# Performance work log

Hardware: AMD Instinct MI355X
Metric: run time of the kernel (lower is better)

## Reference

```python
import jax, jax.numpy as jnp
import numpy as np

D_MODEL = 1024
N_HEADS = 16
D_HEAD = 64
GROUP_SIZE = 2
N_GROUPS = N_HEADS // GROUP_SIZE


def setup_inputs() -> dict:
    key = jax.random.key(0)
    k1, k2, k3, k4, k5 = jax.random.split(key, 5)
    def xavier(k, shape):
        fan_in, fan_out = shape[0], int(np.prod(shape[1:]))
        bound = float(np.sqrt(6.0 / (fan_in + fan_out)))
        return jax.random.uniform(k, shape, jnp.float32, -bound, bound)
    return {
        'resid': jax.random.normal(k1, (2, 2048, D_MODEL), jnp.float32),
        'W_Q': xavier(k2, (D_MODEL, N_HEADS, D_HEAD)),
        'W_K': xavier(k3, (D_MODEL, N_GROUPS, D_HEAD)),
        'W_V': xavier(k4, (D_MODEL, N_GROUPS, D_HEAD)),
        'W_out': xavier(k5, (D_HEAD, N_HEADS, D_MODEL)),
        'b_out': jnp.zeros((D_MODEL,), jnp.float32),
    }


def reference(resid, W_Q, W_K, W_V, W_out, b_out):
    batch, seq, _ = resid.shape
    # q: [b, s, n_heads, d_head] -> [b, s, n_groups, group_size, d_head]
    q = jnp.einsum('bsd,dhe->bshe', resid, W_Q)
    q = q.reshape(batch, seq, N_GROUPS, GROUP_SIZE, D_HEAD)
    k = jnp.einsum('bsd,dge->bsge', resid, W_K)  # [b, s, g, e]
    v = jnp.einsum('bsd,dge->bsge', resid, W_V)
    # scores: [b, g, group_size, qseq, kseq]
    scores = jnp.einsum('bqgre,bkge->bgrqk', q, k) / jnp.sqrt(jnp.float32(D_HEAD))
    causal_mask = jnp.triu(jnp.ones((seq, seq), bool), k=1)
    scores = jnp.where(causal_mask, jnp.float32(-1000000.0), scores)
    probs = jax.nn.softmax(scores, axis=-1)
    # z: [b, q, g, r, e]
    z = jnp.einsum('bgrqk,bkge->bqgre', probs, v)
    z = z.reshape(batch, seq, N_HEADS, D_HEAD)
    out = jnp.einsum('bshe,ehd->bsd', z, W_out) + b_out
    return out
```

## Files before the change

kernel.cpp:

```cpp
#include <hip/hip_runtime.h>

#define BATCH   2
#define SEQ     2048
#define DMODEL  1024
#define NHEADS  16
#define DHEAD   64
#define NGROUPS 8
#define NTOK    (BATCH * SEQ)
#define QKV_N   2048

typedef unsigned short ushort_t;
typedef unsigned int u32;
typedef __attribute__((ext_vector_type(8))) short short8;
typedef __attribute__((ext_vector_type(4))) float f32x4;
typedef __attribute__((ext_vector_type(16))) float f32x16;

#define MFMA16(a, b, c) __builtin_amdgcn_mfma_f32_16x16x32_bf16((a), (b), (c), 0, 0, 0)
#define MFMA32(a, b, c) __builtin_amdgcn_mfma_f32_32x32x16_bf16((a), (b), (c), 0, 0, 0)

#define GLOAD16(gp, lp)                                                        \
    __builtin_amdgcn_global_load_lds(                                          \
        (const u32 __attribute__((address_space(1)))*)(gp),                    \
        (u32 __attribute__((address_space(3)))*)(lp), 16, 0, 0)

#define CVTPK(dst, lo, hi) \
    asm("v_cvt_pk_bf16_f32 %0, %1, %2" : "=v"(dst) : "v"(lo), "v"(hi))

#define PLSWAP(a, b) \
    asm("v_permlane32_swap_b32 %0, %1" : "+v"(a), "+v"(b))

__device__ __forceinline__ ushort_t f2bu(float x) {
    unsigned u = __builtin_bit_cast(unsigned, x);
    unsigned r = (u + 0x7fffu + ((u >> 16) & 1u)) >> 16;
    return (ushort_t)r;
}

__global__ __launch_bounds__(256) void prep(
    const float* __restrict__ resid,
    const float* __restrict__ Wq, const float* __restrict__ Wk,
    const float* __restrict__ Wv, const float* __restrict__ Wout,
    ushort_t* __restrict__ rbf, ushort_t* __restrict__ Wt,
    ushort_t* __restrict__ Wot)
{
    __shared__ float Ws[64][65];
    const int t = threadIdx.x;
    const int bid = blockIdx.x;

    if (bid < 4096) {
        const int i4 = bid * 256 + t;
        union { float4 v; float f[4]; } a;
        a.v = *reinterpret_cast<const float4*>(resid + (size_t)i4 * 4);
        union { uint2 v; ushort_t u[4]; } o;
        #pragma unroll
        for (int j = 0; j < 4; ++j) o.u[j] = f2bu(a.f[j]);
        *reinterpret_cast<uint2*>(rbf + (size_t)i4 * 4) = o.v;
        return;
    }

    if (bid < 4096 + 512) {
        const int rel = bid - 4096;
        const int k0 = (rel & 15) * 64;
        const int n0 = (rel >> 4) * 64;

        const float* src; int stride, boff;
        if (n0 < 1024)       { src = Wq; stride = 1024; boff = n0; }
        else if (n0 < 1536)  { src = Wk; stride = 512;  boff = n0 - 1024; }
        else                 { src = Wv; stride = 512;  boff = n0 - 1536; }

        #pragma unroll
        for (int i = 0; i < 4; ++i) {
            const int c = i * 256 + t;
            const int row = c >> 4, cc = (c & 15) * 4;
            union { float4 v; float f[4]; } a;
            a.v = *reinterpret_cast<const float4*>(
                src + (size_t)(k0 + row) * stride + boff + cc);
            #pragma unroll
            for (int j = 0; j < 4; ++j) Ws[row][cc + j] = a.f[j];
        }
        __syncthreads();
        #pragma unroll
        for (int i = 0; i < 2; ++i) {
            const int c = i * 256 + t;
            const int nr = c >> 3, kc = (c & 7) * 8;
            union { uint4 v; ushort_t u[8]; } o;
            #pragma unroll
            for (int j = 0; j < 8; ++j) o.u[j] = f2bu(Ws[kc + j][nr]);
            *reinterpret_cast<uint4*>(Wt + (size_t)(n0 + nr) * 1024 + k0 + kc) = o.v;
        }
        return;
    }

    {
        const int rel = bid - 4608;
        const int d0 = (rel & 15) * 64;
        const int h  = rel >> 4;

        #pragma unroll
        for (int i = 0; i < 4; ++i) {
            const int c = i * 256 + t;
            const int e = c >> 4, dd = (c & 15) * 4;
            union { float4 v; float f[4]; } a;
            a.v = *reinterpret_cast<const float4*>(
                Wout + (size_t)(e * 16 + h) * 1024 + d0 + dd);
            #pragma unroll
            for (int j = 0; j < 4; ++j) Ws[e][dd + j] = a.f[j];
        }
        __syncthreads();
        #pragma unroll
        for (int i = 0; i < 2; ++i) {
            const int c = i * 256 + t;
            const int dr = c >> 3, ec = (c & 7) * 8;
            union { uint4 v; ushort_t u[8]; } o;
            #pragma unroll
            for (int j = 0; j < 8; ++j) o.u[j] = f2bu(Ws[ec + j][dr]);
            *reinterpret_cast<uint4*>(Wot + (size_t)(d0 + dr) * 1024 + h * 64 + ec) = o.v;
        }
    }
}

__global__ __launch_bounds__(256) void tr_v(
    const ushort_t* __restrict__ qkv, ushort_t* __restrict__ Vt)
{
    __shared__ ushort_t T[64][72];
    const int t  = threadIdx.x;
    const int s0 = blockIdx.x * 64;
    const int g  = blockIdx.y;
    const int b  = blockIdx.z;

    #pragma unroll
    for (int i = 0; i < 2; ++i) {
        const int c = i * 256 + t;
        const int row = c >> 3, ec = (c & 7) * 8;
        *reinterpret_cast<uint4*>(&T[row][ec]) =
            *reinterpret_cast<const uint4*>(
                qkv + (size_t)(b * SEQ + s0 + row) * QKV_N + 1536 + g * 64 + ec);
    }
    __syncthreads();
    #pragma unroll
    for (int i = 0; i < 2; ++i) {
        const int c = i * 256 + t;
        const int er = c >> 3, sc = (c & 7) * 8;
        union { uint4 v; ushort_t u[8]; } o;
        #pragma unroll
        for (int j = 0; j < 8; ++j) o.u[j] = T[sc + j][er];
        *reinterpret_cast<uint4*>(
            Vt + (size_t)((b * NGROUPS + g) * 64 + er) * SEQ + s0 + sc) = o.v;
    }
}

__global__ __launch_bounds__(512) void qkv_gemm(
    const ushort_t* __restrict__ A, const ushort_t* __restrict__ Bt,
    ushort_t* __restrict__ C)
{
    __shared__ ushort_t As[2][128][64];
    __shared__ ushort_t Bs[2][128][64];

    const int t = threadIdx.x;
    const int wave = t >> 6, lane = t & 63;
    const int quad = lane >> 4, x = lane & 15;
    const int wm = (wave >> 1) * 32, wn = (wave & 1) * 64;
    const int m0 = blockIdx.y * 128, n0 = blockIdx.x * 128;

    const int sr8 = lane >> 3;
    const int gc  = (lane & 7) ^ sr8;

    f32x4 acc[2][4];
    #pragma unroll
    for (int i = 0; i < 2; ++i)
        #pragma unroll
        for (int j = 0; j < 4; ++j) acc[i][j] = (f32x4)(0.f);

    #pragma unroll
    for (int s = 0; s < 2; ++s) {
        const int r0 = (wave * 2 + s) * 8;
        GLOAD16(A  + (size_t)(m0 + r0 + sr8) * 1024 + gc * 8, &As[0][r0][0]);
        GLOAD16(Bt + (size_t)(n0 + r0 + sr8) * 1024 + gc * 8, &Bs[0][r0][0]);
    }
    __syncthreads();

    int cur = 0;
    for (int k0 = 0; k0 < 1024; k0 += 64) {
        if (k0 + 64 < 1024) {
            #pragma unroll
            for (int s = 0; s < 2; ++s) {
                const int r0 = (wave * 2 + s) * 8;
                GLOAD16(A  + (size_t)(m0 + r0 + sr8) * 1024 + k0 + 64 + gc * 8,
                        &As[cur ^ 1][r0][0]);
                GLOAD16(Bt + (size_t)(n0 + r0 + sr8) * 1024 + k0 + 64 + gc * 8,
                        &Bs[cur ^ 1][r0][0]);
            }
        }
        #pragma unroll
        for (int j = 0; j < 2; ++j) {
            const int cs = ((j * 4 + quad) ^ (x & 7)) * 8;
            short8 af[2], bf[4];
            #pragma unroll
            for (int mt = 0; mt < 2; ++mt)
                af[mt] = *reinterpret_cast<const short8*>(&As[cur][wm + mt * 16 + x][cs]);
            #pragma unroll
            for (int nt = 0; nt < 4; ++nt)
                bf[nt] = *reinterpret_cast<const short8*>(&Bs[cur][wn + nt * 16 + x][cs]);
            #pragma unroll
            for (int mt = 0; mt < 2; ++mt)
                #pragma unroll
                for (int nt = 0; nt < 4; ++nt)
                    acc[mt][nt] = MFMA16(af[mt], bf[nt], acc[mt][nt]);
        }
        __syncthreads();
        cur ^= 1;
    }

    #pragma unroll
    for (int mt = 0; mt < 2; ++mt)
        #pragma unroll
        for (int nt = 0; nt < 4; ++nt)
            #pragma unroll
            for (int r = 0; r < 4; ++r) {
                const int row = m0 + wm + mt * 16 + quad * 4 + r;
                const int col = n0 + wn + nt * 16 + x;
                C[(size_t)row * QKV_N + col] = f2bu(acc[mt][nt][r]);
            }
}

__global__ __launch_bounds__(512) void out_gemm(
    const ushort_t* __restrict__ A, const ushort_t* __restrict__ Bt,
    const float* __restrict__ bias, float* __restrict__ C)
{
    __shared__ ushort_t As[2][128][64];
    __shared__ ushort_t Bs[2][64][64];

    const int t = threadIdx.x;
    const int wave = t >> 6, lane = t & 63;
    const int quad = lane >> 4, x = lane & 15;
    const int wm = (wave >> 1) * 32, wn = (wave & 1) * 32;
    const int m0 = blockIdx.y * 128, n0 = blockIdx.x * 64;

    const int sr8 = lane >> 3;
    const int gc  = (lane & 7) ^ sr8;

    f32x4 acc[2][2];
    #pragma unroll
    for (int i = 0; i < 2; ++i)
        #pragma unroll
        for (int j = 0; j < 2; ++j) acc[i][j] = (f32x4)(0.f);

    #pragma unroll
    for (int s = 0; s < 2; ++s) {
        const int r0 = (wave * 2 + s) * 8;
        GLOAD16(A + (size_t)(m0 + r0 + sr8) * 1024 + gc * 8, &As[0][r0][0]);
    }
    {
        const int r0 = wave * 8;
        GLOAD16(Bt + (size_t)(n0 + r0 + sr8) * 1024 + gc * 8, &Bs[0][r0][0]);
    }
    __syncthreads();

    int cur = 0;
    for (int k0 = 0; k0 < 1024; k0 += 64) {
        if (k0 + 64 < 1024) {
            #pragma unroll
            for (int s = 0; s < 2; ++s) {
                const int r0 = (wave * 2 + s) * 8;
                GLOAD16(A + (size_t)(m0 + r0 + sr8) * 1024 + k0 + 64 + gc * 8,
                        &As[cur ^ 1][r0][0]);
            }
            const int r0 = wave * 8;
            GLOAD16(Bt + (size_t)(n0 + r0 + sr8) * 1024 + k0 + 64 + gc * 8,
                    &Bs[cur ^ 1][r0][0]);
        }
        #pragma unroll
        for (int j = 0; j < 2; ++j) {
            const int cs = ((j * 4 + quad) ^ (x & 7)) * 8;
            short8 af[2], bf[2];
            #pragma unroll
            for (int mt = 0; mt < 2; ++mt)
                af[mt] = *reinterpret_cast<const short8*>(&As[cur][wm + mt * 16 + x][cs]);
            #pragma unroll
            for (int nt = 0; nt < 2; ++nt)
                bf[nt] = *reinterpret_cast<const short8*>(&Bs[cur][wn + nt * 16 + x][cs]);
            #pragma unroll
            for (int mt = 0; mt < 2; ++mt)
                #pragma unroll
                for (int nt = 0; nt < 2; ++nt)
                    acc[mt][nt] = MFMA16(af[mt], bf[nt], acc[mt][nt]);
        }
        __syncthreads();
        cur ^= 1;
    }

    float bv[2];
    #pragma unroll
    for (int nt = 0; nt < 2; ++nt) bv[nt] = bias[n0 + wn + nt * 16 + x];

    #pragma unroll
    for (int mt = 0; mt < 2; ++mt)
        #pragma unroll
        for (int nt = 0; nt < 2; ++nt)
            #pragma unroll
            for (int r = 0; r < 4; ++r) {
                const int row = m0 + wm + mt * 16 + quad * 4 + r;
                const int col = n0 + wn + nt * 16 + x;
                C[(size_t)row * 1024 + col] = acc[mt][nt][r] + bv[nt];
            }
}

__global__ __launch_bounds__(512, 4) void attn(
    const ushort_t* __restrict__ qkv, const ushort_t* __restrict__ Vt,
    ushort_t* __restrict__ z)
{
    __shared__ ushort_t smem[4 * 128 * 64];
    ushort_t (*Ks)[128][64]  = (ushort_t(*)[128][64])(smem);
    ushort_t (*Vts)[64][128] = (ushort_t(*)[64][128])(smem + 2 * 128 * 64);
    float* Ob1  = (float*)smem;
    float* Ob3  = (float*)(smem + 128 * 64);
    float* Ofin = (float*)(smem + 2 * 128 * 64);
    float* Lb1  = (float*)(smem + 3 * 128 * 64);
    float* Lb3  = Lb1 + 64;

    const int t = threadIdx.x;
    const int wave = t >> 6, lane = t & 63;
    const int x31 = lane & 31, hi = lane >> 5;
    const int rw = wave & 1;
    const int kw = wave >> 1;

    const int h  = blockIdx.x;
    const int qp = blockIdx.y;
    const int b  = blockIdx.z;
    const int g  = h >> 1;

    const int krow = t >> 3;
    const int kc   = t & 7;
    const int vrow = t >> 4;
    const int vc   = t & 15;

    const ushort_t* kgb = qkv + (size_t)(b * SEQ) * QKV_N + 1024 + g * 64 + kc * 8;
    const ushort_t* vgb = Vt + (size_t)((b * NGROUPS + g) * 64) * SEQ + vc * 8;

    const int kswz = (kc ^ (krow & 7)) * 8;
    const int vswz = (vc ^ (vrow & 15)) * 8;

    const int qloc = rw * 32 + x31;

    #pragma unroll
    for (int phase = 0; phase < 2; ++phase) {
        const int qt = phase ? (31 - qp) : qp;
        const int qrow0 = qt * 64;
        const int nkt = (qt >> 1) + 1;

        short8 aq[4];
        #pragma unroll
        for (int sl = 0; sl < 4; ++sl)
            aq[sl] = *reinterpret_cast<const short8*>(
                qkv + (size_t)(b * SEQ + qrow0 + qloc) * QKV_N + h * 64 + sl * 16 + hi * 8);

        f32x16 o0 = (f32x16)(0.f), o1 = (f32x16)(0.f);
        float lown = 0.f;

        __syncthreads();

        {
            uint4 a0 = *reinterpret_cast<const uint4*>(kgb + (size_t)krow * QKV_N);
            uint4 a1 = *reinterpret_cast<const uint4*>(kgb + (size_t)(krow + 64) * QKV_N);
            uint4 b0 = *reinterpret_cast<const uint4*>(vgb + (size_t)vrow * SEQ);
            uint4 b1 = *reinterpret_cast<const uint4*>(vgb + (size_t)(vrow + 32) * SEQ);
            *reinterpret_cast<uint4*>(&Ks[0][krow][kswz])       = a0;
            *reinterpret_cast<uint4*>(&Ks[0][krow + 64][kswz])  = a1;
            *reinterpret_cast<uint4*>(&Vts[0][vrow][vswz])      = b0;
            *reinterpret_cast<uint4*>(&Vts[0][vrow + 32][vswz]) = b1;
        }
        __syncthreads();

        for (int kt = 0; kt < nkt; ++kt) {
            const int cur = kt & 1;
            const bool more = (kt + 1 < nkt);

            uint4 a0, a1, b0, b1;
            if (more) {
                const size_t kb = (size_t)((kt + 1) * 128);
                a0 = *reinterpret_cast<const uint4*>(kgb + (kb + krow) * QKV_N);
                a1 = *reinterpret_cast<const uint4*>(kgb + (kb + krow + 64) * QKV_N);
                b0 = *reinterpret_cast<const uint4*>(vgb + (size_t)vrow * SEQ + kb);
                b1 = *reinterpret_cast<const uint4*>(vgb + (size_t)(vrow + 32) * SEQ + kb);
            }

            const int cbase = kt * 128 + kw * 32;
            const int qmin  = qrow0 + rw * 32;

            if (cbase <= qmin + 31) {
                const bool full = (cbase + 31 <= qmin);

                f32x16 st = (f32x16)(0.f);
                __builtin_amdgcn_s_setprio(1);
                #pragma unroll
                for (int sl = 0; sl < 4; ++sl) {
                    short8 ak = *reinterpret_cast<const short8*>(
                        &Ks[cur][kw * 32 + x31][((sl * 2 + hi) ^ (x31 & 7)) * 8]);
                    st = MFMA32(ak, aq[sl], st);
                }
                __builtin_amdgcn_s_setprio(0);

                const int ql = qmin + x31 - cbase;
                float p[16];
                float s16 = 0.f;
                #pragma unroll
                for (int r = 0; r < 16; ++r) {
                    const int keyoff = (r & 3) + 8 * (r >> 2);
                    float pv = __expf(st[r] * 0.125f);
                    if (!full) pv = (keyoff + 4 * hi > ql) ? 0.f : pv;
                    p[r] = pv;
                    s16 += pv;
                }
                lown += s16;

                u32 pk0, pk1, pk2, pk3, pk4, pk5, pk6, pk7;
                CVTPK(pk0, p[0],  p[1]);  CVTPK(pk1, p[2],  p[3]);
                CVTPK(pk2, p[4],  p[5]);  CVTPK(pk3, p[6],  p[7]);
                CVTPK(pk4, p[8],  p[9]);  CVTPK(pk5, p[10], p[11]);
                CVTPK(pk6, p[12], p[13]); CVTPK(pk7, p[14], p[15]);
                PLSWAP(pk0, pk2); PLSWAP(pk1, pk3);
                PLSWAP(pk4, pk6); PLSWAP(pk5, pk7);
                union { u32 u[4]; short8 s; } f0, f1;
                f0.u[0] = pk0; f0.u[1] = pk1; f0.u[2] = pk2; f0.u[3] = pk3;
                f1.u[0] = pk4; f1.u[1] = pk5; f1.u[2] = pk6; f1.u[3] = pk7;

                __builtin_amdgcn_s_setprio(1);
                #pragma unroll
                for (int ks = 0; ks < 2; ++ks) {
                    const short8 pf = ks ? f1.s : f0.s;
                    short8 av0 = *reinterpret_cast<const short8*>(
                        &Vts[cur][x31][((kw * 4 + ks * 2 + hi) ^ (x31 & 15)) * 8]);
                    o0 = MFMA32(av0, pf, o0);
                    short8 av1 = *reinterpret_cast<const short8*>(
                        &Vts[cur][32 + x31][((kw * 4 + ks * 2 + hi) ^ (x31 & 15)) * 8]);
                    o1 = MFMA32(av1, pf, o1);
                }
                __builtin_amdgcn_s_setprio(0);
            }

            if (more) {
                *reinterpret_cast<uint4*>(&Ks[cur ^ 1][krow][kswz])       = a0;
                *reinterpret_cast<uint4*>(&Ks[cur ^ 1][krow + 64][kswz])  = a1;
                *reinterpret_cast<uint4*>(&Vts[cur ^ 1][vrow][vswz])      = b0;
                *reinterpret_cast<uint4*>(&Vts[cur ^ 1][vrow + 32][vswz]) = b1;
            }
            __syncthreads();
        }

        float ltot;
        {
            u32 la = __builtin_bit_cast(u32, lown), lb = la;
            PLSWAP(la, lb);
            const float lpart = __builtin_bit_cast(float, hi ? la : lb);
            ltot = lown + lpart;
        }

        if (kw == 1 || kw == 3) {
            float* Obx = (kw == 1) ? Ob1 : Ob3;
            float* Lbx = (kw == 1) ? Lb1 : Lb3;
            #pragma unroll
            for (int r = 0; r < 16; ++r) {
                const int e = (r & 3) + 8 * (r >> 2) + 4 * hi;
                Obx[e * 64 + qloc]        = o0[r];
                Obx[(32 + e) * 64 + qloc] = o1[r];
            }
            if (hi == 0) Lbx[qloc] = ltot;
        }
        __syncthreads();
        if (kw == 0 || kw == 2) {
            const float* Obx = (kw == 0) ? Ob1 : Ob3;
            const float* Lbx = (kw == 0) ? Lb1 : Lb3;
            #pragma unroll
            for (int r = 0; r < 16; ++r) {
                const int e = (r & 3) + 8 * (r >> 2) + 4 * hi;
                o0[r] += Obx[e * 64 + qloc];
                o1[r] += Obx[(32 + e) * 64 + qloc];
            }
            ltot += Lbx[qloc];
        }
        __syncthreads();
        if (kw == 2) {
            #pragma unroll
            for (int r = 0; r < 16; ++r) {
                const int e = (r & 3) + 8 * (r >> 2) + 4 * hi;
                Ob1[e * 64 + qloc]        = o0[r];
                Ob1[(32 + e) * 64 + qloc] = o1[r];
            }
            if (hi == 0) Lb1[qloc] = ltot;
        }
        __syncthreads();
        if (kw == 0) {
            #pragma unroll
            for (int r = 0; r < 16; ++r) {
                const int e = (r & 3) + 8 * (r >> 2) + 4 * hi;
                o0[r] += Ob1[e * 64 + qloc];
                o1[r] += Ob1[(32 + e) * 64 + qloc];
            }
            ltot += Lb1[qloc];
            const float inv = 1.f / ltot;
            #pragma unroll
            for (int r = 0; r < 16; ++r) {
                const int e = (r & 3) + 8 * (r >> 2) + 4 * hi;
                Ofin[e * 64 + qloc]        = o0[r] * inv;
                Ofin[(32 + e) * 64 + qloc] = o1[r] * inv;
            }
        }
        __syncthreads();

        {
            const int q = t >> 3, ec = t & 7;
            union { u32 u[4]; uint4 v; } pkz;
            #pragma unroll
            for (int j2 = 0; j2 < 4; ++j2) {
                float v0 = Ofin[(ec * 8 + 2 * j2) * 64 + q];
                float v1 = Ofin[(ec * 8 + 2 * j2 + 1) * 64 + q];
                CVTPK(pkz.u[j2], v0, v1);
            }
            *reinterpret_cast<uint4*>(
                z + (size_t)(b * SEQ + qrow0 + q) * 1024 + h * 64 + ec * 8) = pkz.v;
        }
    }
}

extern "C" void kernel_launch(void* const* d_in, const int* in_sizes, int n_in,
                              void* d_out, int out_size, void* d_ws, size_t ws_size,
                              hipStream_t stream)
{
    const float* resid = (const float*)d_in[0];
    const float* Wq    = (const float*)d_in[1];
    const float* Wk    = (const float*)d_in[2];
    const float* Wv    = (const float*)d_in[3];
    const float* Wout  = (const float*)d_in[4];
    const float* bout  = (const float*)d_in[5];
    float* out = (float*)d_out;

    ushort_t* rbf   = (ushort_t*)d_ws;
    ushort_t* wqkvt = rbf   + (size_t)NTOK * DMODEL;
    ushort_t* woutt = wqkvt + (size_t)QKV_N * DMODEL;
    ushort_t* qkv   = woutt + (size_t)DMODEL * DMODEL;
    ushort_t* z     = qkv   + (size_t)NTOK * QKV_N;
    ushort_t* vt    = rbf;

    prep     <<<dim3(4864), 256, 0, stream>>>(resid, Wq, Wk, Wv, Wout,
                                              rbf, wqkvt, woutt);
    qkv_gemm <<<dim3(16, 32), 512, 0, stream>>>(rbf, wqkvt, qkv);
    tr_v     <<<dim3(SEQ / 64, NGROUPS, BATCH), 256, 0, stream>>>(qkv, vt);
    attn     <<<dim3(16, 16, 2), 512, 0, stream>>>(qkv, vt, z);
    out_gemm <<<dim3(16, 32), 512, 0, stream>>>(z, woutt, bout, out);
}
```

Baseline: 164.5 us.

## Load K/V fragments directly from global memory instead of staging through LDS

The attention kernel no longer stages K and V tiles through double-buffered shared memory with per-tile barriers. Each wave now loads its own K and V MFMA fragments straight from global memory into registers and skips masked tiles early. This removes LDS traffic and the __syncthreads per key tile. In exchange, fragments shared across waves are fetched redundantly from global/L2, and there is no explicit prefetch to hide load latency.

```diff
diff --git a/kernel.cpp b/kernel.cpp
--- a/kernel.cpp
+++ b/kernel.cpp
@@ -308,14 +308,11 @@
     const ushort_t* __restrict__ qkv, const ushort_t* __restrict__ Vt,
     ushort_t* __restrict__ z)
 {
-    __shared__ ushort_t smem[4 * 128 * 64];
-    ushort_t (*Ks)[128][64]  = (ushort_t(*)[128][64])(smem);
-    ushort_t (*Vts)[64][128] = (ushort_t(*)[64][128])(smem + 2 * 128 * 64);
-    float* Ob1  = (float*)smem;
-    float* Ob3  = (float*)(smem + 128 * 64);
-    float* Ofin = (float*)(smem + 2 * 128 * 64);
-    float* Lb1  = (float*)(smem + 3 * 128 * 64);
-    float* Lb3  = Lb1 + 64;
+    __shared__ float Ob1[64 * 64];
+    __shared__ float Ob3[64 * 64];
+    __shared__ float Ofin[64 * 64];
+    __shared__ float Lb1[64];
+    __shared__ float Lb3[64];
 
     const int t = threadIdx.x;
     const int wave = t >> 6, lane = t & 63;
@@ -328,16 +325,8 @@
     const int b  = blockIdx.z;
     const int g  = h >> 1;
 
-    const int krow = t >> 3;
-    const int kc   = t & 7;
-    const int vrow = t >> 4;
-    const int vc   = t & 15;
-
-    const ushort_t* kgb = qkv + (size_t)(b * SEQ) * QKV_N + 1024 + g * 64 + kc * 8;
-    const ushort_t* vgb = Vt + (size_t)((b * NGROUPS + g) * 64) * SEQ + vc * 8;
-
-    const int kswz = (kc ^ (krow & 7)) * 8;
-    const int vswz = (vc ^ (vrow & 15)) * 8;
+    const ushort_t* kg = qkv + (size_t)(b * SEQ) * QKV_N + 1024 + g * 64;
+    const ushort_t* vg = Vt + (size_t)((b * NGROUPS + g) * 64) * SEQ;
 
     const int qloc = rw * 32 + x31;
 
@@ -356,94 +345,67 @@
         f32x16 o0 = (f32x16)(0.f), o1 = (f32x16)(0.f);
         float lown = 0.f;
 
-        __syncthreads();
-
-        {
-            uint4 a0 = *reinterpret_cast<const uint4*>(kgb + (size_t)krow * QKV_N);
-            uint4 a1 = *reinterpret_cast<const uint4*>(kgb + (size_t)(krow + 64) * QKV_N);
-            uint4 b0 = *reinterpret_cast<const uint4*>(vgb + (size_t)vrow * SEQ);
-            uint4 b1 = *reinterpret_cast<const uint4*>(vgb + (size_t)(vrow + 32) * SEQ);
-            *reinterpret_cast<uint4*>(&Ks[0][krow][kswz])       = a0;
-            *reinterpret_cast<uint4*>(&Ks[0][krow + 64][kswz])  = a1;
-            *reinterpret_cast<uint4*>(&Vts[0][vrow][vswz])      = b0;
-            *reinterpret_cast<uint4*>(&Vts[0][vrow + 32][vswz]) = b1;
-        }
-        __syncthreads();
-
         for (int kt = 0; kt < nkt; ++kt) {
-            const int cur = kt & 1;
-            const bool more = (kt + 1 < nkt);
-
-            uint4 a0, a1, b0, b1;
-            if (more) {
-                const size_t kb = (size_t)((kt + 1) * 128);
-                a0 = *reinterpret_cast<const uint4*>(kgb + (kb + krow) * QKV_N);
-                a1 = *reinterpret_cast<const uint4*>(kgb + (kb + krow + 64) * QKV_N);
-                b0 = *reinterpret_cast<const uint4*>(vgb + (size_t)vrow * SEQ + kb);
-                b1 = *reinterpret_cast<const uint4*>(vgb + (size_t)(vrow + 32) * SEQ + kb);
-            }
-
             const int cbase = kt * 128 + kw * 32;
             const int qmin  = qrow0 + rw * 32;
-
-            if (cbase <= qmin + 31) {
-                const bool full = (cbase + 31 <= qmin);
-
-                f32x16 st = (f32x16)(0.f);
-                __builtin_amdgcn_s_setprio(1);
-                #pragma unroll
-                for (int sl = 0; sl < 4; ++sl) {
-                    short8 ak = *reinterpret_cast<const short8*>(
-                        &Ks[cur][kw * 32 + x31][((sl * 2 + hi) ^ (x31 & 7)) * 8]);
-                    st = MFMA32(ak, aq[sl], st);
-                }
-                __builtin_amdgcn_s_setprio(0);
-
-                const int ql = qmin + x31 - cbase;
-                float p[16];
-                float s16 = 0.f;
-                #pragma unroll
-                for (int r = 0; r < 16; ++r) {
-                    const int keyoff = (r & 3) + 8 * (r >> 2);
-                    float pv = __expf(st[r] * 0.125f);
-                    if (!full) pv = (keyoff + 4 * hi > ql) ? 0.f : pv;
-                    p[r] = pv;
-                    s16 += pv;
-                }
-                lown += s16;
-
-                u32 pk0, pk1, pk2, pk3, pk4, pk5, pk6, pk7;
-                CVTPK(pk0, p[0],  p[1]);  CVTPK(pk1, p[2],  p[3]);
-                CVTPK(pk2, p[4],  p[5]);  CVTPK(pk3, p[6],  p[7]);
-                CVTPK(pk4, p[8],  p[9]);  CVTPK(pk5, p[10], p[11]);
-                CVTPK(pk6, p[12], p[13]); CVTPK(pk7, p[14], p[15]);
-                PLSWAP(pk0, pk2); PLSWAP(pk1, pk3);
-                PLSWAP(pk4, pk6); PLSWAP(pk5, pk7);
-                union { u32 u[4]; short8 s; } f0, f1;
-                f0.u[0] = pk0; f0.u[1] = pk1; f0.u[2] = pk2; f0.u[3] = pk3;
-                f1.u[0] = pk4; f1.u[1] = pk5; f1.u[2] = pk6; f1.u[3] = pk7;
-
-                __builtin_amdgcn_s_setprio(1);
-                #pragma unroll
-                for (int ks = 0; ks < 2; ++ks) {
-                    const short8 pf = ks ? f1.s : f0.s;
-                    short8 av0 = *reinterpret_cast<const short8*>(
-                        &Vts[cur][x31][((kw * 4 + ks * 2 + hi) ^ (x31 & 15)) * 8]);
-                    o0 = MFMA32(av0, pf, o0);
-                    short8 av1 = *reinterpret_cast<const short8*>(
-                        &Vts[cur][32 + x31][((kw * 4 + ks * 2 + hi) ^ (x31 & 15)) * 8]);
-                    o1 = MFMA32(av1, pf, o1);
-                }
-                __builtin_amdgcn_s_setprio(0);
-            }
-
-            if (more) {
-                *reinterpret_cast<uint4*>(&Ks[cur ^ 1][krow][kswz])       = a0;
-                *reinterpret_cast<uint4*>(&Ks[cur ^ 1][krow + 64][kswz])  = a1;
-                *reinterpret_cast<uint4*>(&Vts[cur ^ 1][vrow][vswz])      = b0;
-                *reinterpret_cast<uint4*>(&Vts[cur ^ 1][vrow + 32][vswz]) = b1;
-            }
-            __syncthreads();
+            if (cbase > qmin + 31) continue;
+            const bool full = (cbase + 31 <= qmin);
+
+            short8 kf[4];
+            #pragma unroll
+            for (int sl = 0; sl < 4; ++sl)
+                kf[sl] = *reinterpret_cast<const short8*>(
+                    kg + (size_t)(cbase + x31) * QKV_N + sl * 16 + hi * 8);
+
+            short8 vf0[2], vf1[2];
+            #pragma unroll
+            for (int ks = 0; ks < 2; ++ks) {
+                const size_t vcol = (size_t)(kt * 128 + (kw * 4 + ks * 2 + hi) * 8);
+                vf0[ks] = *reinterpret_cast<const short8*>(
+                    vg + (size_t)x31 * SEQ + vcol);
+                vf1[ks] = *reinterpret_cast<const short8*>(
+                    vg + (size_t)(32 + x31) * SEQ + vcol);
+            }
+
+            f32x16 st = (f32x16)(0.f);
+            __builtin_amdgcn_s_setprio(1);
+            #pragma unroll
+            for (int sl = 0; sl < 4; ++sl)
+                st = MFMA32(kf[sl], aq[sl], st);
+            __builtin_amdgcn_s_setprio(0);
+
+            const int ql = qmin + x31 - cbase;
+            float p[16];
+            float s16 = 0.f;
+            #pragma unroll
+            for (int r = 0; r < 16; ++r) {
+                const int keyoff = (r & 3) + 8 * (r >> 2);
+                float pv = __expf(st[r] * 0.125f);
+                if (!full) pv = (keyoff + 4 * hi > ql) ? 0.f : pv;
+                p[r] = pv;
+                s16 += pv;
+            }
+            lown += s16;
+
+            u32 pk0, pk1, pk2, pk3, pk4, pk5, pk6, pk7;
+            CVTPK(pk0, p[0],  p[1]);  CVTPK(pk1, p[2],  p[3]);
+            CVTPK(pk2, p[4],  p[5]);  CVTPK(pk3, p[6],  p[7]);
+            CVTPK(pk4, p[8],  p[9]);  CVTPK(pk5, p[10], p[11]);
+            CVTPK(pk6, p[12], p[13]); CVTPK(pk7, p[14], p[15]);
+            PLSWAP(pk0, pk2); PLSWAP(pk1, pk3);
+            PLSWAP(pk4, pk6); PLSWAP(pk5, pk7);
+            union { u32 u[4]; short8 s; } f0, f1;
+            f0.u[0] = pk0; f0.u[1] = pk1; f0.u[2] = pk2; f0.u[3] = pk3;
+            f1.u[0] = pk4; f1.u[1] = pk5; f1.u[2] = pk6; f1.u[3] = pk7;
+
+            __builtin_amdgcn_s_setprio(1);
+            #pragma unroll
+            for (int ks = 0; ks < 2; ++ks) {
+                const short8 pf = ks ? f1.s : f0.s;
+                o0 = MFMA32(vf0[ks], pf, o0);
+                o1 = MFMA32(vf1[ks], pf, o1);
+            }
+            __builtin_amdgcn_s_setprio(0);
         }
 
         float ltot;
```

New measurement: 199.3 us. 1.21x slower.
